# Optimization experiments

Hardware: AMD Instinct MI355X
Metric: run time of the kernel (lower is better)

## Reference

```python
import jax, jax.numpy as jnp
import numpy as np

N = 100000      # nodes
E = 1600000     # edges (avg degree 16)
F_IN = 128      # in_feats
H = 128         # n_hidden
C = 40          # n_classes


def setup_inputs() -> dict:
    key = jax.random.key(0)
    ks = jax.random.split(key, 11)
    s = 0.05
    return {
        "x": jax.random.normal(ks[0], (N, F_IN), jnp.float32),
        "edge_index": jax.random.randint(ks[1], (2, E), 0, N, jnp.int32),
        # layer 1: SAGEConv(F_IN, H); lin_l has bias, lin_r has none (PyG default)
        "Wl1": jax.random.normal(ks[2], (F_IN, H), jnp.float32) * s,
        "bl1": jnp.zeros((H,), jnp.float32),
        "Wr1": jax.random.normal(ks[3], (F_IN, H), jnp.float32) * s,
        # layer 2: SAGEConv(H, H)
        "Wl2": jax.random.normal(ks[4], (H, H), jnp.float32) * s,
        "bl2": jnp.zeros((H,), jnp.float32),
        "Wr2": jax.random.normal(ks[5], (H, H), jnp.float32) * s,
        # layer 3: SAGEConv(H, C)
        "Wl3": jax.random.normal(ks[6], (H, C), jnp.float32) * s,
        "bl3": jnp.zeros((C,), jnp.float32),
        "Wr3": jax.random.normal(ks[7], (H, C), jnp.float32) * s,
    }


def _sage_conv(x, src, dst, Wl, bl, Wr):
    # PyG SAGEConv (aggr='mean', root_weight=True):
    #   out[i] = lin_l( mean_{j->i} x[j] ) + lin_r( x[i] )
    msgs = x[src]                                            # [E, d] irregular gather
    agg = jax.ops.segment_sum(msgs, dst, num_segments=N)     # [N, d]
    deg = jax.ops.segment_sum(jnp.ones((src.shape[0], 1), x.dtype), dst,
                              num_segments=N)                # [N, 1]
    agg = agg / jnp.maximum(deg, 1.0)                        # mean aggregation
    return agg @ Wl + bl + x @ Wr


def reference(x, edge_index, Wl1, bl1, Wr1, Wl2, bl2, Wr2, Wl3, bl3, Wr3):
    src, dst = edge_index[0], edge_index[1]
    h = jax.nn.relu(_sage_conv(x, src, dst, Wl1, bl1, Wr1))   # dropout is identity in eval
    h = jax.nn.relu(_sage_conv(h, src, dst, Wl2, bl2, Wr2))
    return _sage_conv(h, src, dst, Wl3, bl3, Wr3)             # [N, C]
```

## Files before the change

### kernel.cpp

```cpp
#include <hip/hip_runtime.h>

using u16 = unsigned short;
using u32 = unsigned int;
using u8 = unsigned char;
typedef __attribute__((ext_vector_type(8))) short short8;
typedef __attribute__((ext_vector_type(4))) float f32x4;

static inline int idiv_up(long a, long b) { return (int)((a + b - 1) / b); }

#define NBUCK 256
#define ECHUNK 8192
#define CAPE 9216

__device__ __forceinline__ float bflo(u32 p) { return __uint_as_float(p << 16); }
__device__ __forceinline__ float bfhi(u32 p) { return __uint_as_float(p & 0xffff0000u); }
__device__ __forceinline__ u32 f2bf1(float f) {
    u32 x = __float_as_uint(f);
    return (x + 0x7fffu + ((x >> 16) & 1u)) >> 16;
}
__device__ __forceinline__ u32 pack2(float lo, float hi) {
    return f2bf1(lo) | (f2bf1(hi) << 16);
}

__global__ __launch_bounds__(256) void k_cast(const float* __restrict__ x,
                                              u32* __restrict__ xb, long nelem) {
    long i = ((long)blockIdx.x * 256 + threadIdx.x) * 8;
    if (i >= nelem) return;
    float4 v0 = *(const float4*)(x + i);
    float4 v1 = *(const float4*)(x + i + 4);
    uint4 o;
    o.x = pack2(v0.x, v0.y);
    o.y = pack2(v0.z, v0.w);
    o.z = pack2(v1.x, v1.y);
    o.w = pack2(v1.z, v1.w);
    *(uint4*)(xb + (i >> 1)) = o;
}

__global__ __launch_bounds__(256) void k_wprep(const float* __restrict__ Wl,
                                               const float* __restrict__ Wr,
                                               u16* __restrict__ wp) {
    const int gid = blockIdx.x * 256 + threadIdx.x;
    if (gid >= 64 * 64) return;
    const int tile = gid >> 6, l = gid & 63;
    const int t = tile >> 3, s = tile & 7;
    const int n = t * 16 + (l & 15);
    const int k0 = s * 32 + (l >> 4) * 8;
    u32 w[4];
#pragma unroll
    for (int p = 0; p < 4; ++p) {
        const int ka = k0 + 2 * p, kb = ka + 1;
        const float va = (ka < 128) ? Wl[ka * 128 + n] : Wr[(ka - 128) * 128 + n];
        const float vb = (kb < 128) ? Wl[kb * 128 + n] : Wr[(kb - 128) * 128 + n];
        w[p] = pack2(va, vb);
    }
    uint4 o = {w[0], w[1], w[2], w[3]};
    *(uint4*)(wp + (size_t)gid * 8) = o;
}

__global__ __launch_bounds__(256) void k_wprep3(const float* __restrict__ Wl,
                                                const float* __restrict__ Wr,
                                                u16* __restrict__ wp) {
    const int gid = blockIdx.x * 256 + threadIdx.x;
    if (gid >= 20 * 64) return;
    const int tile = gid >> 6, l = gid & 63;
    const int t = tile >> 2, s = tile & 3;
    const int c = t * 16 + (l & 15);
    const int k0 = s * 32 + (l >> 4) * 8;
    u32 w[4];
#pragma unroll
    for (int p = 0; p < 4; ++p) {
        const int ka = k0 + 2 * p, kb = ka + 1;
        const float va = (c < 40) ? Wl[ka * 40 + c] : Wr[ka * 40 + (c - 40)];
        const float vb = (c < 40) ? Wl[kb * 40 + c] : Wr[kb * 40 + (c - 40)];
        w[p] = pack2(va, vb);
    }
    uint4 o = {w[0], w[1], w[2], w[3]};
    *(uint4*)(wp + (size_t)gid * 8) = o;
}

__global__ __launch_bounds__(256) void k_bucket(const int* __restrict__ src,
                                                const int* __restrict__ dst,
                                                int* __restrict__ cursor,
                                                u32* __restrict__ stage,
                                                int E, int rangeSize) {
    __shared__ u32 s_pay[ECHUNK];
    __shared__ u8 s_bk[ECHUNK];
    __shared__ int s_cnt[NBUCK];
    __shared__ int s_base[NBUCK];
    __shared__ int s_off[NBUCK];
    s_cnt[threadIdx.x] = 0;
    __syncthreads();
    const long e0 = (long)blockIdx.x * ECHUNK;
    const int cnt = (int)(((long)E - e0 < ECHUNK) ? (long)E - e0 : ECHUNK);
    for (int j = threadIdx.x; j < cnt; j += 256) {
        const int d = __builtin_nontemporal_load(&dst[e0 + j]);
        const int s = __builtin_nontemporal_load(&src[e0 + j]);
        const int b = d / rangeSize;
        s_pay[j] = (u32)s | ((u32)(d - b * rangeSize) << 17);
        s_bk[j] = (u8)b;
        atomicAdd(&s_cnt[b], 1);
    }
    __syncthreads();
    {
        const int c = s_cnt[threadIdx.x];
        s_base[threadIdx.x] = c ? atomicAdd(&cursor[threadIdx.x], c) : 0;
        s_off[threadIdx.x] = 0;
    }
    __syncthreads();
    for (int j = threadIdx.x; j < cnt; j += 256) {
        const int b = s_bk[j];
        const int p = atomicAdd(&s_off[b], 1);
        stage[(size_t)b * CAPE + s_base[b] + p] = s_pay[j];
    }
}

__global__ __launch_bounds__(256) void k_bscan(const int* __restrict__ cursor,
                                               int* __restrict__ bbase, int E) {
    __shared__ int wt[4];
    const int t = threadIdx.x;
    const int v = cursor[t];
    const int lane = t & 63, wid = t >> 6;
    int incl = v;
    for (int off = 1; off < 64; off <<= 1) {
        int u = __shfl_up(incl, off, 64);
        if (lane >= off) incl += u;
    }
    if (lane == 63) wt[wid] = incl;
    __syncthreads();
    int woff = 0;
    for (int w = 0; w < wid; ++w) woff += wt[w];
    bbase[t] = woff + incl - v;
    if (t == 255) bbase[256] = woff + incl;
}

__global__ __launch_bounds__(256) void k_csrlds(const u32* __restrict__ stage,
                                                const int* __restrict__ bcnt,
                                                const int* __restrict__ bbase,
                                                int* __restrict__ rowptr,
                                                float* __restrict__ invd,
                                                int* __restrict__ col,
                                                int rangeSize, int n) {
    __shared__ int s_cnt[512];
    __shared__ int s_cur[512];
    __shared__ int s_col[CAPE];
    __shared__ int wt[4];
    const int b = blockIdx.x;
    const int t = threadIdx.x;
    const int g0 = b * rangeSize;
    const size_t rd = (size_t)b * CAPE;
    const int cntb = bcnt[b];
    const int gbase = bbase[b];

    for (int i = t; i < rangeSize; i += 256) s_cnt[i] = 0;
    __syncthreads();

    for (int i = t; i < cntb; i += 256)
        atomicAdd(&s_cnt[stage[rd + i] >> 17], 1);
    __syncthreads();

    const int i0 = 2 * t, i1 = 2 * t + 1;
    const int c0 = (i0 < rangeSize) ? s_cnt[i0] : 0;
    const int c1 = (i1 < rangeSize) ? s_cnt[i1] : 0;
    const int sum = c0 + c1;
    const int lane = t & 63, wid = t >> 6;
    int incl = sum;
    for (int off = 1; off < 64; off <<= 1) {
        int u = __shfl_up(incl, off, 64);
        if (lane >= off) incl += u;
    }
    if (lane == 63) wt[wid] = incl;
    __syncthreads();
    int woff = 0;
    for (int w = 0; w < wid; ++w) woff += wt[w];
    const int excl = woff + incl - sum;
    if (i0 < rangeSize) {
        s_cur[i0] = excl;
        const int g = g0 + i0;
        if (g <= n) rowptr[g] = gbase + excl;
        if (g < n) invd[g] = 1.0f / fmaxf((float)c0, 1.0f);
    }
    if (i1 < rangeSize) {
        s_cur[i1] = excl + c0;
        const int g = g0 + i1;
        if (g <= n) rowptr[g] = gbase + excl + c0;
        if (g < n) invd[g] = 1.0f / fmaxf((float)c1, 1.0f);
    }
    __syncthreads();

    for (int i = t; i < cntb; i += 256) {
        const u32 v = stage[rd + i];
        const int p = atomicAdd(&s_cur[v >> 17], 1);
        s_col[p] = (int)(v & 0x1FFFFu);
    }
    __syncthreads();

    for (int i = t; i < cntb; i += 256) col[gbase + i] = s_col[i];
}

#define ACC8(A, B, V)                                                          \
    A.x += bflo(V.x); A.y += bfhi(V.x); A.z += bflo(V.y); A.w += bfhi(V.y);    \
    B.x += bflo(V.z); B.y += bfhi(V.z); B.z += bflo(V.w); B.w += bfhi(V.w);

__global__ __launch_bounds__(256) void k_aggb(const u16* __restrict__ xb,
                                              const int* __restrict__ rowptr,
                                              const int* __restrict__ col,
                                              const float* __restrict__ invd,
                                              u16* __restrict__ aggb, int n) {
    const int t = blockIdx.x * 256 + threadIdx.x;
    const int node = t >> 4;
    if (node >= n) return;
    const int l = t & 15;
    const int s0 = rowptr[node], s1 = rowptr[node + 1];
    float4 eA0 = {0.f, 0.f, 0.f, 0.f}, eA1 = {0.f, 0.f, 0.f, 0.f};
    float4 eB0 = {0.f, 0.f, 0.f, 0.f}, eB1 = {0.f, 0.f, 0.f, 0.f};
    for (int cb = s0; cb < s1; cb += 16) {
        const int cnt = min(16, s1 - cb);
        const int cc = (cb + l < s1) ? col[cb + l] : 0;
        int j = 0;
        for (; j + 4 <= cnt; j += 4) {
            const int n0 = __shfl(cc, j, 16);
            const int n1 = __shfl(cc, j + 1, 16);
            const int n2 = __shfl(cc, j + 2, 16);
            const int n3 = __shfl(cc, j + 3, 16);
            const uint4 v0 = *(const uint4*)(xb + (size_t)n0 * 128 + 8 * l);
            const uint4 v1 = *(const uint4*)(xb + (size_t)n1 * 128 + 8 * l);
            const uint4 v2 = *(const uint4*)(xb + (size_t)n2 * 128 + 8 * l);
            const uint4 v3 = *(const uint4*)(xb + (size_t)n3 * 128 + 8 * l);
            ACC8(eA0, eA1, v0); ACC8(eB0, eB1, v1);
            ACC8(eA0, eA1, v2); ACC8(eB0, eB1, v3);
        }
        for (; j < cnt; ++j) {
            const int nn = __shfl(cc, j, 16);
            const uint4 v = *(const uint4*)(xb + (size_t)nn * 128 + 8 * l);
            ACC8(eA0, eA1, v);
        }
    }
    const float inv = invd[node];
    uint4 o;
    o.x = pack2((eA0.x + eB0.x) * inv, (eA0.y + eB0.y) * inv);
    o.y = pack2((eA0.z + eB0.z) * inv, (eA0.w + eB0.w) * inv);
    o.z = pack2((eA1.x + eB1.x) * inv, (eA1.y + eB1.y) * inv);
    o.w = pack2((eA1.z + eB1.z) * inv, (eA1.w + eB1.w) * inv);
    *(uint4*)(aggb + (size_t)node * 128 + 8 * l) = o;
}

__global__ __launch_bounds__(256, 4) void k_mmf(const u16* __restrict__ aggb,
                                                const u16* __restrict__ xrb,
                                                const u16* __restrict__ wp,
                                                const float* __restrict__ bl,
                                                u16* __restrict__ outb, int n) {
    __shared__ __align__(16) u16 s_a[64][264];
    const int row0 = blockIdx.x * 64;
    const int tid = threadIdx.x;

#pragma unroll
    for (int it = 0; it < 8; ++it) {
        const int idx = tid + it * 256;
        const int r = idx >> 5, c8 = idx & 31;
        const int row = row0 + r;
        uint4 v = {0u, 0u, 0u, 0u};
        if (row < n) {
            v = (c8 < 16) ? *(const uint4*)(aggb + (size_t)row * 128 + c8 * 8)
                          : *(const uint4*)(xrb + (size_t)row * 128 + (c8 - 16) * 8);
        }
        *(uint4*)(&s_a[r][c8 * 8]) = v;
    }
    __syncthreads();

    const int l = tid & 63;
    const int w = tid >> 6;
    const int rloc = w * 16 + (l & 15);
    const int q = l >> 4;

    short8 afr[8];
#pragma unroll
    for (int s = 0; s < 8; ++s)
        afr[s] = *(const short8*)(&s_a[rloc][s * 32 + q * 8]);

    f32x4 acc[8];
#pragma unroll
    for (int t = 0; t < 8; ++t) acc[t] = (f32x4){0.f, 0.f, 0.f, 0.f};

#pragma unroll
    for (int t = 0; t < 8; ++t) {
#pragma unroll
        for (int s = 0; s < 8; ++s) {
            const short8 b = *(const short8*)(wp + ((size_t)(t * 8 + s) * 64 + l) * 8);
            acc[t] = __builtin_amdgcn_mfma_f32_16x16x32_bf16(afr[s], b, acc[t], 0, 0, 0);
        }
    }

    const int rowb = row0 + w * 16 + q * 4;
#pragma unroll
    for (int t = 0; t < 8; ++t) {
        const float bias = bl[t * 16 + (l & 15)];
#pragma unroll
        for (int r = 0; r < 4; ++r) {
            const int row = rowb + r;
            if (row < n) {
                const float o = fmaxf(acc[t][r] + bias, 0.f);
                outb[(size_t)row * 128 + t * 16 + (l & 15)] = (u16)f2bf1(o);
            }
        }
    }
}

__global__ __launch_bounds__(256, 4) void k_mm40f(const u16* __restrict__ hb,
                                                  const u16* __restrict__ wp,
                                                  const float* __restrict__ bl,
                                                  u16* __restrict__ t40b,
                                                  float* __restrict__ r40, int n) {
    __shared__ __align__(16) u16 s_a[64][136];
    const int row0 = blockIdx.x * 64;
    const int tid = threadIdx.x;

#pragma unroll
    for (int it = 0; it < 4; ++it) {
        const int idx = tid + it * 256;
        const int r = idx >> 4, c8 = idx & 15;
        const int row = row0 + r;
        uint4 v = {0u, 0u, 0u, 0u};
        if (row < n) v = *(const uint4*)(hb + (size_t)row * 128 + c8 * 8);
        *(uint4*)(&s_a[r][c8 * 8]) = v;
    }
    __syncthreads();

    const int l = tid & 63;
    const int w = tid >> 6;
    const int rloc = w * 16 + (l & 15);
    const int q = l >> 4;

    short8 afr[4];
#pragma unroll
    for (int s = 0; s < 4; ++s)
        afr[s] = *(const short8*)(&s_a[rloc][s * 32 + q * 8]);

    f32x4 acc[5];
#pragma unroll
    for (int t = 0; t < 5; ++t) acc[t] = (f32x4){0.f, 0.f, 0.f, 0.f};

#pragma unroll
    for (int t = 0; t < 5; ++t) {
#pragma unroll
        for (int s = 0; s < 4; ++s) {
            const short8 b = *(const short8*)(wp + ((size_t)(t * 4 + s) * 64 + l) * 8);
            acc[t] = __builtin_amdgcn_mfma_f32_16x16x32_bf16(afr[s], b, acc[t], 0, 0, 0);
        }
    }

    const int rowb = row0 + w * 16 + q * 4;
#pragma unroll
    for (int t = 0; t < 5; ++t) {
        const int c = t * 16 + (l & 15);
        const float bias = (c >= 40) ? bl[c - 40] : 0.f;
#pragma unroll
        for (int r = 0; r < 4; ++r) {
            const int row = rowb + r;
            if (row < n) {
                if (c < 40)
                    t40b[(size_t)row * 40 + c] = (u16)f2bf1(acc[t][r]);
                else
                    r40[(size_t)row * 40 + (c - 40)] = acc[t][r] + bias;
            }
        }
    }
}

#define ACC4(A, V)                                                     \
    A.x += bflo(V.x); A.y += bfhi(V.x); A.z += bflo(V.y); A.w += bfhi(V.y);

__global__ __launch_bounds__(256) void k_agg40(const u16* __restrict__ t40b,
                                               const float* __restrict__ r40,
                                               const int* __restrict__ rowptr,
                                               const int* __restrict__ col,
                                               const float* __restrict__ invd,
                                               float* __restrict__ out, int n) {
    const int tt = blockIdx.x * 256 + threadIdx.x;
    const int node = tt >> 4;
    if (node >= n) return;
    const int l = tt & 15;
    const bool act = l < 10;
    const int s0 = rowptr[node], s1 = rowptr[node + 1];
    float4 a0 = {0.f, 0.f, 0.f, 0.f};
    float4 a1 = {0.f, 0.f, 0.f, 0.f};
    for (int cb = s0; cb < s1; cb += 16) {
        const int cnt = min(16, s1 - cb);
        const int cc = (cb + l < s1) ? col[cb + l] : 0;
        int j = 0;
        for (; j + 4 <= cnt; j += 4) {
            const int n0 = __shfl(cc, j, 16);
            const int n1 = __shfl(cc, j + 1, 16);
            const int n2 = __shfl(cc, j + 2, 16);
            const int n3 = __shfl(cc, j + 3, 16);
            if (act) {
                const uint2 v0 = *(const uint2*)(t40b + (size_t)n0 * 40 + 4 * l);
                const uint2 v1 = *(const uint2*)(t40b + (size_t)n1 * 40 + 4 * l);
                const uint2 v2 = *(const uint2*)(t40b + (size_t)n2 * 40 + 4 * l);
                const uint2 v3 = *(const uint2*)(t40b + (size_t)n3 * 40 + 4 * l);
                ACC4(a0, v0); ACC4(a1, v1); ACC4(a0, v2); ACC4(a1, v3);
            }
        }
        for (; j < cnt; ++j) {
            const int nn = __shfl(cc, j, 16);
            if (act) {
                const uint2 v = *(const uint2*)(t40b + (size_t)nn * 40 + 4 * l);
                ACC4(a0, v);
            }
        }
    }
    if (act) {
        const float inv = invd[node];
        const float4 rv = *(const float4*)(r40 + (size_t)node * 40 + 4 * l);
        float4 o;
        o.x = fmaf(a0.x + a1.x, inv, rv.x);
        o.y = fmaf(a0.y + a1.y, inv, rv.y);
        o.z = fmaf(a0.z + a1.z, inv, rv.z);
        o.w = fmaf(a0.w + a1.w, inv, rv.w);
        *(float4*)(out + (size_t)node * 40 + 4 * l) = o;
    }
}

extern "C" void kernel_launch(void* const* d_in, const int* in_sizes, int n_in,
                              void* d_out, int out_size, void* d_ws, size_t ws_size,
                              hipStream_t stream) {
    const float* x   = (const float*)d_in[0];
    const int*   ei  = (const int*)d_in[1];
    const float* Wl1 = (const float*)d_in[2];
    const float* bl1 = (const float*)d_in[3];
    const float* Wr1 = (const float*)d_in[4];
    const float* Wl2 = (const float*)d_in[5];
    const float* bl2 = (const float*)d_in[6];
    const float* Wr2 = (const float*)d_in[7];
    const float* Wl3 = (const float*)d_in[8];
    const float* bl3 = (const float*)d_in[9];
    const float* Wr3 = (const float*)d_in[10];
    float* out = (float*)d_out;

    const int N = in_sizes[0] / 128;
    const int E = in_sizes[1] / 2;
    const int* src = ei;
    const int* dst = ei + E;

    auto align1k = [](size_t v) { return (v + 1023) & ~(size_t)1023; };
    const size_t NB16 = (size_t)N * 128 * sizeof(u16);

    char* ws = (char*)d_ws;
    size_t off = 0;
    float* invd     = (float*)(ws + off); off += align1k((size_t)N * 4);
    int*   rowptr   = (int*)(ws + off);   off += align1k((size_t)(N + 1) * 4);
    int*   cursor   = (int*)(ws + off);   off += align1k(NBUCK * 4);
    int*   bbase    = (int*)(ws + off);   off += align1k((NBUCK + 1) * 4);
    u16*   wp1      = (u16*)(ws + off);   off += align1k(64 * 1024);
    u16*   wp2      = (u16*)(ws + off);   off += align1k(64 * 1024);
    u16*   wp3      = (u16*)(ws + off);   off += align1k(20 * 1024);
    int*   col      = (int*)(ws + off);   off += align1k((size_t)E * 4);
    u32*   stage    = (u32*)(ws + off);   off += align1k((size_t)NBUCK * CAPE * 4);
    u16*   aggb     = (u16*)(ws + off);   off += align1k(NB16);
    u16*   xb       = (u16*)(ws + off);   off += align1k(NB16);
    char*  regionY  = (ws + off);         off += align1k(NB16);
    u16*   h1b  = (u16*)regionY;
    u16*   h2b  = xb;
    u16*   t40b = (u16*)regionY;
    float* r40  = (float*)(regionY + align1k((size_t)N * 40 * sizeof(u16)));

    const int nPB        = idiv_up(E, ECHUNK);
    const int castBlocks = idiv_up((long)N * 128, 2048);
    const int aggBlocks  = idiv_up((long)N * 16, 256);
    const int agg40Blk   = idiv_up((long)N * 16, 256);
    const int mmBlocks   = idiv_up(N, 64);
    const int rangeSize  = idiv_up(N, NBUCK);

    k_cast<<<castBlocks, 256, 0, stream>>>(x, (u32*)xb, (long)N * 128);
    k_wprep<<<16, 256, 0, stream>>>(Wl1, Wr1, wp1);
    k_wprep<<<16, 256, 0, stream>>>(Wl2, Wr2, wp2);
    k_wprep3<<<5, 256, 0, stream>>>(Wl3, Wr3, wp3);

    hipMemsetAsync(cursor, 0, NBUCK * sizeof(int), stream);
    k_bucket<<<nPB, 256, 0, stream>>>(src, dst, cursor, stage, E, rangeSize);
    k_bscan<<<1, 256, 0, stream>>>(cursor, bbase, E);
    k_csrlds<<<NBUCK, 256, 0, stream>>>(stage, cursor, bbase, rowptr, invd, col,
                                        rangeSize, N);

    k_aggb<<<aggBlocks, 256, 0, stream>>>(xb, rowptr, col, invd, aggb, N);
    k_mmf<<<mmBlocks, 256, 0, stream>>>(aggb, xb, wp1, bl1, h1b, N);

    k_aggb<<<aggBlocks, 256, 0, stream>>>(h1b, rowptr, col, invd, aggb, N);
    k_mmf<<<mmBlocks, 256, 0, stream>>>(aggb, h1b, wp2, bl2, h2b, N);

    k_mm40f<<<mmBlocks, 256, 0, stream>>>(h2b, wp3, bl3, t40b, r40, N);
    k_agg40<<<agg40Blk, 256, 0, stream>>>(t40b, r40, rowptr, col, invd, out, N);
}
```

Baseline: 301.4 us.

## Fuse neighbor mean aggregation into the MFMA matmul kernel for layers one and two

Merges the gather-and-mean aggregation kernel into the matmul kernel, so each 64-row block aggregates its nodes' neighbors straight into shared memory and then runs the MFMA product. This removes the write and re-read of the intermediate aggregated buffer and two kernel launches per pair of layers. In exchange, each thread now walks four nodes in sequence inside a block capped by launch bounds at 4 blocks per CU, which may expose less memory-level parallelism for the irregular gathers than the standalone aggregation kernel had.

```diff
diff --git a/kernel.cpp b/kernel.cpp
--- a/kernel.cpp
+++ b/kernel.cpp
@@ -201,76 +201,67 @@
     A.x += bflo(V.x); A.y += bfhi(V.x); A.z += bflo(V.y); A.w += bfhi(V.y);    \
     B.x += bflo(V.z); B.y += bfhi(V.z); B.z += bflo(V.w); B.w += bfhi(V.w);
 
-__global__ __launch_bounds__(256) void k_aggb(const u16* __restrict__ xb,
-                                              const int* __restrict__ rowptr,
-                                              const int* __restrict__ col,
-                                              const float* __restrict__ invd,
-                                              u16* __restrict__ aggb, int n) {
-    const int t = blockIdx.x * 256 + threadIdx.x;
-    const int node = t >> 4;
-    if (node >= n) return;
-    const int l = t & 15;
-    const int s0 = rowptr[node], s1 = rowptr[node + 1];
-    float4 eA0 = {0.f, 0.f, 0.f, 0.f}, eA1 = {0.f, 0.f, 0.f, 0.f};
-    float4 eB0 = {0.f, 0.f, 0.f, 0.f}, eB1 = {0.f, 0.f, 0.f, 0.f};
-    for (int cb = s0; cb < s1; cb += 16) {
-        const int cnt = min(16, s1 - cb);
-        const int cc = (cb + l < s1) ? col[cb + l] : 0;
-        int j = 0;
-        for (; j + 4 <= cnt; j += 4) {
-            const int n0 = __shfl(cc, j, 16);
-            const int n1 = __shfl(cc, j + 1, 16);
-            const int n2 = __shfl(cc, j + 2, 16);
-            const int n3 = __shfl(cc, j + 3, 16);
-            const uint4 v0 = *(const uint4*)(xb + (size_t)n0 * 128 + 8 * l);
-            const uint4 v1 = *(const uint4*)(xb + (size_t)n1 * 128 + 8 * l);
-            const uint4 v2 = *(const uint4*)(xb + (size_t)n2 * 128 + 8 * l);
-            const uint4 v3 = *(const uint4*)(xb + (size_t)n3 * 128 + 8 * l);
-            ACC8(eA0, eA1, v0); ACC8(eB0, eB1, v1);
-            ACC8(eA0, eA1, v2); ACC8(eB0, eB1, v3);
-        }
-        for (; j < cnt; ++j) {
-            const int nn = __shfl(cc, j, 16);
-            const uint4 v = *(const uint4*)(xb + (size_t)nn * 128 + 8 * l);
-            ACC8(eA0, eA1, v);
-        }
-    }
-    const float inv = invd[node];
-    uint4 o;
-    o.x = pack2((eA0.x + eB0.x) * inv, (eA0.y + eB0.y) * inv);
-    o.y = pack2((eA0.z + eB0.z) * inv, (eA0.w + eB0.w) * inv);
-    o.z = pack2((eA1.x + eB1.x) * inv, (eA1.y + eB1.y) * inv);
-    o.w = pack2((eA1.z + eB1.z) * inv, (eA1.w + eB1.w) * inv);
-    *(uint4*)(aggb + (size_t)node * 128 + 8 * l) = o;
-}
-
-__global__ __launch_bounds__(256, 4) void k_mmf(const u16* __restrict__ aggb,
-                                                const u16* __restrict__ xrb,
-                                                const u16* __restrict__ wp,
-                                                const float* __restrict__ bl,
-                                                u16* __restrict__ outb, int n) {
+__global__ __launch_bounds__(256, 4) void k_aggmm(const u16* __restrict__ xb,
+                                                  const int* __restrict__ rowptr,
+                                                  const int* __restrict__ col,
+                                                  const float* __restrict__ invd,
+                                                  const u16* __restrict__ wp,
+                                                  const float* __restrict__ bl,
+                                                  u16* __restrict__ outb, int n) {
     __shared__ __align__(16) u16 s_a[64][264];
     const int row0 = blockIdx.x * 64;
     const int tid = threadIdx.x;
-
-#pragma unroll
-    for (int it = 0; it < 8; ++it) {
-        const int idx = tid + it * 256;
-        const int r = idx >> 5, c8 = idx & 31;
-        const int row = row0 + r;
-        uint4 v = {0u, 0u, 0u, 0u};
-        if (row < n) {
-            v = (c8 < 16) ? *(const uint4*)(aggb + (size_t)row * 128 + c8 * 8)
-                          : *(const uint4*)(xrb + (size_t)row * 128 + (c8 - 16) * 8);
-        }
-        *(uint4*)(&s_a[r][c8 * 8]) = v;
-    }
-    __syncthreads();
-
-    const int l = tid & 63;
+    const int l = tid & 15;
+
+#pragma unroll
+    for (int it = 0; it < 4; ++it) {
+        const int r = it * 16 + (tid >> 4);
+        const int node = row0 + r;
+        float4 eA0 = {0.f, 0.f, 0.f, 0.f}, eA1 = {0.f, 0.f, 0.f, 0.f};
+        float4 eB0 = {0.f, 0.f, 0.f, 0.f}, eB1 = {0.f, 0.f, 0.f, 0.f};
+        uint4 xv = {0u, 0u, 0u, 0u};
+        float inv = 0.f;
+        if (node < n) {
+            xv = *(const uint4*)(xb + (size_t)node * 128 + 8 * l);
+            inv = invd[node];
+            const int s0 = rowptr[node], s1 = rowptr[node + 1];
+            for (int cb = s0; cb < s1; cb += 16) {
+                const int cnt = min(16, s1 - cb);
+                const int cc = (cb + l < s1) ? col[cb + l] : 0;
+                int j = 0;
+                for (; j + 4 <= cnt; j += 4) {
+                    const int n0 = __shfl(cc, j, 16);
+                    const int n1 = __shfl(cc, j + 1, 16);
+                    const int n2 = __shfl(cc, j + 2, 16);
+                    const int n3 = __shfl(cc, j + 3, 16);
+                    const uint4 v0 = *(const uint4*)(xb + (size_t)n0 * 128 + 8 * l);
+                    const uint4 v1 = *(const uint4*)(xb + (size_t)n1 * 128 + 8 * l);
+                    const uint4 v2 = *(const uint4*)(xb + (size_t)n2 * 128 + 8 * l);
+                    const uint4 v3 = *(const uint4*)(xb + (size_t)n3 * 128 + 8 * l);
+                    ACC8(eA0, eA1, v0); ACC8(eB0, eB1, v1);
+                    ACC8(eA0, eA1, v2); ACC8(eB0, eB1, v3);
+                }
+                for (; j < cnt; ++j) {
+                    const int nn = __shfl(cc, j, 16);
+                    const uint4 v = *(const uint4*)(xb + (size_t)nn * 128 + 8 * l);
+                    ACC8(eA0, eA1, v);
+                }
+            }
+        }
+        uint4 o;
+        o.x = pack2((eA0.x + eB0.x) * inv, (eA0.y + eB0.y) * inv);
+        o.y = pack2((eA0.z + eB0.z) * inv, (eA0.w + eB0.w) * inv);
+        o.z = pack2((eA1.x + eB1.x) * inv, (eA1.y + eB1.y) * inv);
+        o.w = pack2((eA1.z + eB1.z) * inv, (eA1.w + eB1.w) * inv);
+        *(uint4*)(&s_a[r][8 * l]) = o;
+        *(uint4*)(&s_a[r][128 + 8 * l]) = xv;
+    }
+    __syncthreads();
+
+    const int l64 = tid & 63;
     const int w = tid >> 6;
-    const int rloc = w * 16 + (l & 15);
-    const int q = l >> 4;
+    const int rloc = w * 16 + (l64 & 15);
+    const int q = l64 >> 4;
 
     short8 afr[8];
 #pragma unroll
@@ -285,7 +276,7 @@
     for (int t = 0; t < 8; ++t) {
 #pragma unroll
         for (int s = 0; s < 8; ++s) {
-            const short8 b = *(const short8*)(wp + ((size_t)(t * 8 + s) * 64 + l) * 8);
+            const short8 b = *(const short8*)(wp + ((size_t)(t * 8 + s) * 64 + l64) * 8);
             acc[t] = __builtin_amdgcn_mfma_f32_16x16x32_bf16(afr[s], b, acc[t], 0, 0, 0);
         }
     }
@@ -293,13 +284,13 @@
     const int rowb = row0 + w * 16 + q * 4;
 #pragma unroll
     for (int t = 0; t < 8; ++t) {
-        const float bias = bl[t * 16 + (l & 15)];
+        const float bias = bl[t * 16 + (l64 & 15)];
 #pragma unroll
         for (int r = 0; r < 4; ++r) {
             const int row = rowb + r;
             if (row < n) {
                 const float o = fmaxf(acc[t][r] + bias, 0.f);
-                outb[(size_t)row * 128 + t * 16 + (l & 15)] = (u16)f2bf1(o);
+                outb[(size_t)row * 128 + t * 16 + (l64 & 15)] = (u16)f2bf1(o);
             }
         }
     }
@@ -455,7 +446,6 @@
     u16*   wp3      = (u16*)(ws + off);   off += align1k(20 * 1024);
     int*   col      = (int*)(ws + off);   off += align1k((size_t)E * 4);
     u32*   stage    = (u32*)(ws + off);   off += align1k((size_t)NBUCK * CAPE * 4);
-    u16*   aggb     = (u16*)(ws + off);   off += align1k(NB16);
     u16*   xb       = (u16*)(ws + off);   off += align1k(NB16);
     char*  regionY  = (ws + off);         off += align1k(NB16);
     u16*   h1b  = (u16*)regionY;
@@ -465,7 +455,6 @@
 
     const int nPB        = idiv_up(E, ECHUNK);
     const int castBlocks = idiv_up((long)N * 128, 2048);
-    const int aggBlocks  = idiv_up((long)N * 16, 256);
     const int agg40Blk   = idiv_up((long)N * 16, 256);
     const int mmBlocks   = idiv_up(N, 64);
     const int rangeSize  = idiv_up(N, NBUCK);
@@ -481,11 +470,9 @@
     k_csrlds<<<NBUCK, 256, 0, stream>>>(stage, cursor, bbase, rowptr, invd, col,
                                         rangeSize, N);
 
-    k_aggb<<<aggBlocks, 256, 0, stream>>>(xb, rowptr, col, invd, aggb, N);
-    k_mmf<<<mmBlocks, 256, 0, stream>>>(aggb, xb, wp1, bl1, h1b, N);
-
-    k_aggb<<<aggBlocks, 256, 0, stream>>>(h1b, rowptr, col, invd, aggb, N);
-    k_mmf<<<mmBlocks, 256, 0, stream>>>(aggb, h1b, wp2, bl2, h2b, N);
+    k_aggmm<<<mmBlocks, 256, 0, stream>>>(xb, rowptr, col, invd, wp1, bl1, h1b, N);
+
+    k_aggmm<<<mmBlocks, 256, 0, stream>>>(h1b, rowptr, col, invd, wp2, bl2, h2b, N);
 
     k_mm40f<<<mmBlocks, 256, 0, stream>>>(h2b, wp3, bl3, t40b, r40, N);
     k_agg40<<<agg40Blk, 256, 0, stream>>>(t40b, r40, rowptr, col, invd, out, N);
```

After: 291.1 us. -3.4%, faster.
